# Kernel optimization log

Measured on AMD Instinct MI355X. Metric: run time of the kernel, lower is better.

The kernel has to match this reference:

```python
import jax, jax.numpy as jnp
import numpy as np

NUM_HEADS = 12
HEAD_DIM = 64
DIM = NUM_HEADS * HEAD_DIM  # 768
WIN = 14
REL = 2 * WIN - 1  # 27


def setup_inputs() -> dict:
    key = jax.random.key(0)
    ks = jax.random.split(key, 7)
    B, N = 256, WIN * WIN
    return {
        "x": jax.random.normal(ks[0], (B, N, DIM), dtype=jnp.float32),
        "qkv_w": jax.random.normal(ks[1], (3 * DIM, DIM), dtype=jnp.float32) * 0.02,
        "qkv_b": jnp.zeros((3 * DIM,), dtype=jnp.float32),
        "rel_pos_h": jax.random.normal(ks[2], (REL, HEAD_DIM), dtype=jnp.float32) * 0.02,
        "rel_pos_w": jax.random.normal(ks[3], (REL, HEAD_DIM), dtype=jnp.float32) * 0.02,
        "proj_w": jax.random.normal(ks[4], (DIM, DIM), dtype=jnp.float32) * 0.02,
        "proj_b": jnp.zeros((DIM,), dtype=jnp.float32),
        "H": WIN,
        "W": WIN,
    }


def _rel_pos_bias(q, rel_pos_h, rel_pos_w, H, W):
    # q: [B, heads, H*W, d] (already scaled). q_shape == k_shape == (H, W), ratios == 1.
    dist_h = jnp.arange(H)[:, None] - jnp.arange(H)[None, :] + (H - 1)  # [H, H]
    dist_w = jnp.arange(W)[:, None] - jnp.arange(W)[None, :] + (W - 1)  # [W, W]
    Rh = rel_pos_h[dist_h]  # [H, H, d]
    Rw = rel_pos_w[dist_w]  # [W, W, d]
    B, nh = q.shape[0], q.shape[1]
    r_q = q.reshape(B, nh, H, W, q.shape[-1])
    rel_h = jnp.einsum("bnhwd,hkd->bnhwk", r_q, Rh)  # [B, nh, H, W, Hk]
    rel_w = jnp.einsum("bnhwd,wkd->bnhwk", r_q, Rw)  # [B, nh, H, W, Wk]
    return rel_h[..., :, None] + rel_w[..., None, :]  # [B, nh, H, W, Hk, Wk]


def reference(x, qkv_w, qkv_b, rel_pos_h, rel_pos_w, proj_w, proj_b, H, W):
    B, N, C = x.shape
    d = C // NUM_HEADS
    scale = d ** -0.5
    qkv = x @ qkv_w.T + qkv_b  # [B, N, 3C]
    qkv = qkv.reshape(B, N, 3, NUM_HEADS, d).transpose(2, 0, 3, 1, 4)
    q, k, v = qkv[0], qkv[1], qkv[2]  # [B, nh, N, d]
    q = q * scale
    attn = jnp.einsum("bhqd,bhkd->bhqk", q, k)  # [B, nh, N, N]
    bias = _rel_pos_bias(q, rel_pos_h, rel_pos_w, H, W)
    attn = (attn.reshape(B, NUM_HEADS, H, W, H, W) + bias).reshape(B, NUM_HEADS, N, N)
    attn = jax.nn.softmax(attn, axis=-1)
    out = jnp.einsum("bhqk,bhkd->bhqd", attn, v)  # [B, nh, N, d]
    out = out.transpose(0, 2, 1, 3).reshape(B, N, C)
    return out @ proj_w.T + proj_b
```

## Files before the change

kernel.cpp:

```cpp
#include <hip/hip_runtime.h>
#include <stdint.h>


typedef __attribute__((ext_vector_type(8))) short bf16x8;
typedef __attribute__((ext_vector_type(4))) float f32x4;
typedef __attribute__((ext_vector_type(4))) unsigned int u32x4;
typedef unsigned short u16;
typedef unsigned int u32;

__device__ __forceinline__ u16 f2bf(float f) {
  u32 x = __float_as_uint(f);
  x += 0x7fffu + ((x >> 16) & 1u);
  return (u16)(x >> 16);
}

__device__ __forceinline__ u32 pack2bf(float a, float b) {
  return (u32)f2bf(a) | ((u32)f2bf(b) << 16);
}

__device__ __forceinline__ void gload_lds16(const void* g, void* l) {
  __builtin_amdgcn_global_load_lds(
      (__attribute__((address_space(1))) void*)g,
      (__attribute__((address_space(3))) void*)l, 16, 0, 0);
}

__global__ __launch_bounds__(256) void cvt_bf16(const float* __restrict__ src,
                                                u16* __restrict__ dst, int n4) {
  int i = blockIdx.x * 256 + threadIdx.x;
  if (i < n4) {
    float4 f = ((const float4*)src)[i];
    uint2 p;
    p.x = pack2bf(f.x, f.y);
    p.y = pack2bf(f.z, f.w);
    ((uint2*)dst)[i] = p;
  }
}

__device__ __forceinline__ void stage8(const u16* pA, const u16* pB,
                                       char* dstA, int k0) {
#pragma unroll
  for (int i = 0; i < 4; i++)
    gload_lds16(pA + (size_t)i * 49152 + k0, dstA + i * 8192);
#pragma unroll
  for (int i = 0; i < 4; i++)
    gload_lds16(pB + (size_t)i * 49152 + k0, dstA + 32768 + i * 8192);
}

template <int MODE, int NT>
__global__ __launch_bounds__(512, 2) void gemm256(
    const u16* __restrict__ A, const u16* __restrict__ W,
    const float* __restrict__ bias, u16* __restrict__ qb, u16* __restrict__ kb,
    u16* __restrict__ vb, float* __restrict__ outf) {
  __shared__ char lds[131072];

  const int t = threadIdx.x;
  const int lane = t & 63, wv = t >> 6;
  const int quad = lane >> 4, l15 = lane & 15;
  const int wm = wv >> 2, wn = wv & 3;

  const u32 nwg = gridDim.x;
  const u32 wg = blockIdx.x;
  const u32 qd = nwg >> 3, rm = nwg & 7;
  const u32 xcd = wg & 7, loc = wg >> 3;
  const u32 swz = (xcd < rm) ? (xcd * (qd + 1) + loc)
                             : (rm * (qd + 1) + (xcd - rm) * qd + loc);
  const int mtile = swz / NT;
  const int ntile = (int)swz - mtile * NT;
  const int m0 = mtile << 8, n0 = ntile << 8;

  const int srow = t >> 3;
  const int scol = ((t & 7) ^ (srow & 7)) << 3;
  const u16* pA = A + (size_t)(m0 + srow) * 768 + scol;
  const u16* pB = W + (size_t)(n0 + srow) * 768 + scol;
  char* sdst = lds + t * 16;

  const int swz0 = ((quad) ^ (l15 & 7)) << 4;
  const int swz1 = ((4 + quad) ^ (l15 & 7)) << 4;
  const int arow = (wm * 128 + l15) * 128;
  const int brow = 32768 + (wn * 64 + l15) * 128;

  f32x4 acc[8][4];
#pragma unroll
  for (int i = 0; i < 8; i++)
#pragma unroll
    for (int j = 0; j < 4; j++) acc[i][j] = (f32x4){0.f, 0.f, 0.f, 0.f};

  stage8(pA, pB, sdst, 0);
  asm volatile("s_waitcnt vmcnt(0)" ::: "memory");
  __builtin_amdgcn_s_barrier();

  bf16x8 af[4][2], bfr[4][2];
  for (int kt = 0; kt < 12; ++kt) {
    char* bufc = lds + ((kt & 1) << 16);
    char* nsdst = sdst + (((kt & 1) ^ 1) << 16);
    const int k0n = (kt + 1) << 6;

#pragma unroll
    for (int mf = 0; mf < 4; mf++) {
      af[mf][0] = *(const bf16x8*)(bufc + arow + mf * 2048 + swz0);
      af[mf][1] = *(const bf16x8*)(bufc + arow + mf * 2048 + swz1);
    }
#pragma unroll
    for (int nf = 0; nf < 2; nf++) {
      bfr[nf][0] = *(const bf16x8*)(bufc + brow + nf * 2048 + swz0);
      bfr[nf][1] = *(const bf16x8*)(bufc + brow + nf * 2048 + swz1);
    }
    if (kt < 11) stage8(pA, pB, nsdst, k0n);
    __builtin_amdgcn_s_barrier();
    asm volatile("s_waitcnt lgkmcnt(0)" ::: "memory");
    __builtin_amdgcn_s_setprio(1);
#pragma unroll
    for (int k = 0; k < 2; k++)
#pragma unroll
      for (int mf = 0; mf < 4; mf++)
#pragma unroll
        for (int nf = 0; nf < 2; nf++)
          acc[mf][nf] = __builtin_amdgcn_mfma_f32_16x16x32_bf16(
              af[mf][k], bfr[nf][k], acc[mf][nf], 0, 0, 0);
    __builtin_amdgcn_s_setprio(0);
    __builtin_amdgcn_s_barrier();

#pragma unroll
    for (int nf = 2; nf < 4; nf++) {
      bfr[nf][0] = *(const bf16x8*)(bufc + brow + nf * 2048 + swz0);
      bfr[nf][1] = *(const bf16x8*)(bufc + brow + nf * 2048 + swz1);
    }
    __builtin_amdgcn_s_barrier();
    asm volatile("s_waitcnt lgkmcnt(0)" ::: "memory");
    __builtin_amdgcn_s_setprio(1);
#pragma unroll
    for (int k = 0; k < 2; k++)
#pragma unroll
      for (int mf = 0; mf < 4; mf++)
#pragma unroll
        for (int nf = 2; nf < 4; nf++)
          acc[mf][nf] = __builtin_amdgcn_mfma_f32_16x16x32_bf16(
              af[mf][k], bfr[nf][k], acc[mf][nf], 0, 0, 0);
    __builtin_amdgcn_s_setprio(0);
    __builtin_amdgcn_s_barrier();

#pragma unroll
    for (int mf = 0; mf < 4; mf++) {
      af[mf][0] = *(const bf16x8*)(bufc + arow + (mf + 4) * 2048 + swz0);
      af[mf][1] = *(const bf16x8*)(bufc + arow + (mf + 4) * 2048 + swz1);
    }
    __builtin_amdgcn_s_barrier();
    asm volatile("s_waitcnt lgkmcnt(0)" ::: "memory");
    __builtin_amdgcn_s_setprio(1);
#pragma unroll
    for (int k = 0; k < 2; k++)
#pragma unroll
      for (int mf = 0; mf < 4; mf++)
#pragma unroll
        for (int nf = 0; nf < 2; nf++)
          acc[mf + 4][nf] = __builtin_amdgcn_mfma_f32_16x16x32_bf16(
              af[mf][k], bfr[nf][k], acc[mf + 4][nf], 0, 0, 0);
    __builtin_amdgcn_s_setprio(0);
    __builtin_amdgcn_s_barrier();

    __builtin_amdgcn_s_setprio(1);
#pragma unroll
    for (int k = 0; k < 2; k++)
#pragma unroll
      for (int mf = 0; mf < 4; mf++)
#pragma unroll
        for (int nf = 2; nf < 4; nf++)
          acc[mf + 4][nf] = __builtin_amdgcn_mfma_f32_16x16x32_bf16(
              af[mf][k], bfr[nf][k], acc[mf + 4][nf], 0, 0, 0);
    __builtin_amdgcn_s_setprio(0);
    asm volatile("s_waitcnt vmcnt(0)" ::: "memory");
    __builtin_amdgcn_s_barrier();
  }

  if (MODE == 0) {
    const int which = n0 / 768;
    u16* dst = (which == 0) ? qb : ((which == 1) ? kb : vb);
    const float sc = (which == 0) ? 0.125f : 1.0f;
    float bs[4];
    size_t hb[4];
#pragma unroll
    for (int nf = 0; nf < 4; nf++) {
      int n = n0 + wn * 64 + nf * 16 + l15;
      int cc = n - which * 768;
      bs[nf] = bias[n];
      hb[nf] = (size_t)(cc >> 6) * 12544 + (size_t)(cc & 63);
    }
#pragma unroll
    for (int mf = 0; mf < 8; mf++) {
#pragma unroll
      for (int r = 0; r < 4; r++) {
        int m = m0 + wm * 128 + mf * 16 + (quad << 2) + r;
        int bb = m / 196;
        int tok = m - bb * 196;
        size_t rb = (size_t)bb * 150528 + (size_t)tok * 64;
#pragma unroll
        for (int nf = 0; nf < 4; nf++)
          dst[rb + hb[nf]] = f2bf((acc[mf][nf][r] + bs[nf]) * sc);
      }
    }
  } else {
    float bs[4];
#pragma unroll
    for (int nf = 0; nf < 4; nf++)
      bs[nf] = bias[n0 + wn * 64 + nf * 16 + l15];
#pragma unroll
    for (int mf = 0; mf < 8; mf++) {
#pragma unroll
      for (int r = 0; r < 4; r++) {
        int m = m0 + wm * 128 + mf * 16 + (quad << 2) + r;
#pragma unroll
        for (int nf = 0; nf < 4; nf++)
          outf[(size_t)m * 768 + (n0 + wn * 64 + nf * 16 + l15)] =
              acc[mf][nf][r] + bs[nf];
      }
    }
  }
}

__global__ __launch_bounds__(256) void attn_fused(
    const u16* __restrict__ qbuf, const u16* __restrict__ kbuf,
    const u16* __restrict__ vbuf, const float* __restrict__ rel_h,
    const float* __restrict__ rel_w, u16* __restrict__ aout) {
  __shared__ u16 Vt[26 * 512];
  __shared__ float TL[4][2][28][16];

  const int t = threadIdx.x;
  const int bh = blockIdx.x;
  const int b = bh / 12, h = bh - b * 12;
  const int lane = t & 63, wv = t >> 6;
  const int quad = lane >> 4, l15 = lane & 15;
  const size_t base = (size_t)bh * (196 * 64);

  for (int c = t; c < 196 * 8; c += 256) {
    int row = c >> 3, seg = c & 7;
    uint4 vv = *(const uint4*)(vbuf + base + row * 64 + seg * 8);
    const u16* pv8 = (const u16*)&vv;
    u16* dst = Vt + (row >> 3) * 512 + (row & 7);
#pragma unroll
    for (int e = 0; e < 8; e++) dst[(seg * 8 + e) * 8] = pv8[e];
  }
  for (int i = t; i < 12 * 64; i += 256) {
    int k = 196 + (i >> 6), d = i & 63;
    Vt[(k >> 3) * 512 + d * 8 + (k & 7)] = 0;
  }

  bf16x8 brl[2][2][2];
#pragma unroll
  for (int half = 0; half < 2; half++) {
    const float* relp = half ? rel_w : rel_h;
#pragma unroll
    for (int nt = 0; nt < 2; nt++) {
      int ridx = nt * 16 + l15;
      if (ridx > 26) ridx = 26;
#pragma unroll
      for (int ks = 0; ks < 2; ks++) {
        const float* p = relp + ridx * 64 + ks * 32 + quad * 8;
        float4 f0 = *(const float4*)p;
        float4 f1 = *(const float4*)(p + 4);
        bf16x8 r;
        r[0] = (short)f2bf(f0.x); r[1] = (short)f2bf(f0.y);
        r[2] = (short)f2bf(f0.z); r[3] = (short)f2bf(f0.w);
        r[4] = (short)f2bf(f1.x); r[5] = (short)f2bf(f1.y);
        r[6] = (short)f2bf(f1.z); r[7] = (short)f2bf(f1.w);
        brl[half][nt][ks] = r;
      }
    }
  }
  __syncthreads();

  float (*TLh)[16] = TL[wv][0];
  float (*TLw)[16] = TL[wv][1];
  const u16* kB = kbuf + base;
  const u16* qB = qbuf + base;

  for (int qt = wv; qt < 13; qt += 4) {
    int qrl = qt * 16 + l15;
    if (qrl > 195) qrl = 195;
    bf16x8 aq0 = *(const bf16x8*)(qB + qrl * 64 + quad * 8);
    bf16x8 aq1 = *(const bf16x8*)(qB + qrl * 64 + 32 + quad * 8);
    const int hq = qrl / 14, wq = qrl - hq * 14;

#pragma unroll
    for (int half = 0; half < 2; half++) {
#pragma unroll
      for (int nt = 0; nt < 2; nt++) {
        f32x4 tc = (f32x4){0.f, 0.f, 0.f, 0.f};
        tc = __builtin_amdgcn_mfma_f32_16x16x32_bf16(brl[half][nt][0], aq0, tc, 0, 0, 0);
        tc = __builtin_amdgcn_mfma_f32_16x16x32_bf16(brl[half][nt][1], aq1, tc, 0, 0, 0);
#pragma unroll
        for (int r = 0; r < 4; r++) {
          int r27 = nt * 16 + quad * 4 + r;
          if (r27 < 27) TL[wv][half][r27][l15] = tc[r];
        }
      }
    }

    u32 pw2[13][2];
    float sm = 0.f;
#pragma unroll
    for (int kt = 0; kt < 13; kt++) {
      int keyl = kt * 16 + l15;
      int keyc = (keyl > 195) ? 195 : keyl;
      bf16x8 bk0 = *(const bf16x8*)(kB + keyc * 64 + quad * 8);
      bf16x8 bk1 = *(const bf16x8*)(kB + keyc * 64 + 32 + quad * 8);
      f32x4 s = (f32x4){0.f, 0.f, 0.f, 0.f};
      s = __builtin_amdgcn_mfma_f32_16x16x32_bf16(bk0, aq0, s, 0, 0, 0);
      s = __builtin_amdgcn_mfma_f32_16x16x32_bf16(bk1, aq1, s, 0, 0, 0);
      const int key0 = kt * 16 + quad * 4;
      const int hk0 = key0 / 14, wk0 = key0 - 14 * hk0;
      const bool valid = (kt < 12) || (quad == 0);
      float pr[4];
#pragma unroll
      for (int r = 0; r < 4; r++) {
        int cr = (wk0 + r >= 14) ? 1 : 0;
        int hk = hk0 + cr, wk = wk0 + r - 14 * cr;
        float v = s[r] + TLh[hq - hk + 13][l15] + TLw[wq - wk + 13][l15];
        float p = valid ? __expf(v) : 0.f;
        pr[r] = p;
        sm += p;
      }
      pw2[kt][0] = pack2bf(pr[0], pr[1]);
      pw2[kt][1] = pack2bf(pr[2], pr[3]);
    }
    sm += __shfl_xor(sm, 16, 64);
    sm += __shfl_xor(sm, 32, 64);
    const float inv = 1.0f / sm;

    f32x4 oacc[4];
#pragma unroll
    for (int dt = 0; dt < 4; dt++) oacc[dt] = (f32x4){0.f, 0.f, 0.f, 0.f};
    const int srcA = l15 + ((quad & 1) << 5);
    const bool hi = (quad >> 1) != 0;
#pragma unroll
    for (int st = 0; st < 7; st++) {
      u32 w0, w1, w2, w3;
      if (st < 6) {
        u32 a0 = __shfl(pw2[2 * st][0], srcA), b0 = __shfl(pw2[2 * st + 1][0], srcA);
        u32 a1 = __shfl(pw2[2 * st][1], srcA), b1 = __shfl(pw2[2 * st + 1][1], srcA);
        u32 a2 = __shfl(pw2[2 * st][0], srcA + 16), b2 = __shfl(pw2[2 * st + 1][0], srcA + 16);
        u32 a3 = __shfl(pw2[2 * st][1], srcA + 16), b3 = __shfl(pw2[2 * st + 1][1], srcA + 16);
        w0 = hi ? b0 : a0; w1 = hi ? b1 : a1;
        w2 = hi ? b2 : a2; w3 = hi ? b3 : a3;
      } else {
        u32 a0 = __shfl(pw2[12][0], srcA);
        u32 a1 = __shfl(pw2[12][1], srcA);
        u32 a2 = __shfl(pw2[12][0], srcA + 16);
        u32 a3 = __shfl(pw2[12][1], srcA + 16);
        w0 = hi ? 0u : a0; w1 = hi ? 0u : a1;
        w2 = hi ? 0u : a2; w3 = hi ? 0u : a3;
      }
      u32x4 pbw = (u32x4){w0, w1, w2, w3};
      bf16x8 pb = __builtin_bit_cast(bf16x8, pbw);
      const bool mvalid = (st < 6) || (quad < 2);
#pragma unroll
      for (int dt = 0; dt < 4; dt++) {
        bf16x8 av = (bf16x8){0, 0, 0, 0, 0, 0, 0, 0};
        if (mvalid)
          av = *(const bf16x8*)(Vt + (st * 4 + quad) * 512 + (dt * 16 + l15) * 8);
        oacc[dt] = __builtin_amdgcn_mfma_f32_16x16x32_bf16(av, pb, oacc[dt], 0, 0, 0);
      }
    }

    const int qrow = qt * 16 + l15;
    if (qrow < 196) {
      u16* op = aout + ((size_t)(b * 196 + qrow) * 12 + h) * 64;
#pragma unroll
      for (int dt = 0; dt < 4; dt++) {
        uint2 stv;
        stv.x = pack2bf(oacc[dt][0] * inv, oacc[dt][1] * inv);
        stv.y = pack2bf(oacc[dt][2] * inv, oacc[dt][3] * inv);
        *(uint2*)(op + dt * 16 + quad * 4) = stv;
      }
    }
  }
}

extern "C" void kernel_launch(void* const* d_in, const int* in_sizes, int n_in,
                              void* d_out, int out_size, void* d_ws, size_t ws_size,
                              hipStream_t stream) {
  (void)in_sizes; (void)n_in; (void)out_size; (void)ws_size;
  const float* x      = (const float*)d_in[0];
  const float* qkv_w  = (const float*)d_in[1];
  const float* qkv_b  = (const float*)d_in[2];
  const float* rel_h  = (const float*)d_in[3];
  const float* rel_w  = (const float*)d_in[4];
  const float* proj_w = (const float*)d_in[5];
  const float* proj_b = (const float*)d_in[6];
  float* out = (float*)d_out;

  char* ws = (char*)d_ws;
  u16* xbf  = (u16*)(ws);
  u16* qbuf = (u16*)(ws + 77070336);
  u16* kbuf = (u16*)(ws + 154140672);
  u16* vbuf = (u16*)(ws + 231211008);
  u16* wqb  = (u16*)(ws + 308281344);
  u16* wpb  = (u16*)(ws + 311820288);

  cvt_bf16<<<37632, 256, 0, stream>>>(x, xbf, 38535168 / 4);
  cvt_bf16<<<1728, 256, 0, stream>>>(qkv_w, wqb, 1769472 / 4);
  cvt_bf16<<<576, 256, 0, stream>>>(proj_w, wpb, 589824 / 4);

  gemm256<0, 9><<<1764, 512, 0, stream>>>(xbf, wqb, qkv_b, qbuf, kbuf, vbuf,
                                          nullptr);
  attn_fused<<<3072, 256, 0, stream>>>(qbuf, kbuf, vbuf, rel_h, rel_w, xbf);
  gemm256<1, 3><<<588, 512, 0, stream>>>(xbf, wpb, proj_b, nullptr, nullptr,
                                         nullptr, out);
}
```

Baseline: 991.3 us.

## Interleave score/exp with PV MFMA per key pair and rotate V transpose stores

Restructures the attention inner loop so each pair of 16-key tiles is scored, exponentiated, shuffled and immediately multiplied into the output accumulator. The old code first held all 13 tiles of packed probabilities in registers. This cuts the live register footprint (pw2[13][2]) and lets the score MFMAs overlap with the PV MFMAs. The last partial tile is peeled out with index clamping. Separately, the V transpose into LDS rotates the element order by segment, which is meant to reduce LDS bank conflicts on the scattered stores.

```diff
diff --git a/kernel.cpp b/kernel.cpp
--- a/kernel.cpp
+++ b/kernel.cpp
@@ -237,7 +237,10 @@
     const u16* pv8 = (const u16*)&vv;
     u16* dst = Vt + (row >> 3) * 512 + (row & 7);
 #pragma unroll
-    for (int e = 0; e < 8; e++) dst[(seg * 8 + e) * 8] = pv8[e];
+    for (int e = 0; e < 8; e++) {
+      int ee = (e + seg) & 7;
+      dst[(seg * 8 + ee) * 8] = pv8[ee];
+    }
   }
   for (int i = t; i < 12 * 64; i += 256) {
     int k = 196 + (i >> 6), d = i & 63;
@@ -295,71 +298,98 @@
       }
     }
 
-    u32 pw2[13][2];
+    f32x4 oacc[4];
+#pragma unroll
+    for (int dt = 0; dt < 4; dt++) oacc[dt] = (f32x4){0.f, 0.f, 0.f, 0.f};
     float sm = 0.f;
-#pragma unroll
-    for (int kt = 0; kt < 13; kt++) {
-      int keyl = kt * 16 + l15;
-      int keyc = (keyl > 195) ? 195 : keyl;
+    const int srcA = l15 + ((quad & 1) << 5);
+    const bool hi = (quad >> 1) != 0;
+
+#pragma unroll 2
+    for (int st = 0; st < 6; st++) {
+      u32 pw[2][2];
+#pragma unroll
+      for (int u = 0; u < 2; u++) {
+        const int kt = st * 2 + u;
+        const int keyl = kt * 16 + l15;
+        bf16x8 bk0 = *(const bf16x8*)(kB + keyl * 64 + quad * 8);
+        bf16x8 bk1 = *(const bf16x8*)(kB + keyl * 64 + 32 + quad * 8);
+        f32x4 s = (f32x4){0.f, 0.f, 0.f, 0.f};
+        s = __builtin_amdgcn_mfma_f32_16x16x32_bf16(bk0, aq0, s, 0, 0, 0);
+        s = __builtin_amdgcn_mfma_f32_16x16x32_bf16(bk1, aq1, s, 0, 0, 0);
+        const int key0 = kt * 16 + quad * 4;
+        const int hk0 = key0 / 14, wk0 = key0 - 14 * hk0;
+        float pr[4];
+#pragma unroll
+        for (int r = 0; r < 4; r++) {
+          int cr = (wk0 + r >= 14) ? 1 : 0;
+          int hk = hk0 + cr, wk = wk0 + r - 14 * cr;
+          float v = s[r] + TLh[hq - hk + 13][l15] + TLw[wq - wk + 13][l15];
+          float p = __expf(v);
+          pr[r] = p;
+          sm += p;
+        }
+        pw[u][0] = pack2bf(pr[0], pr[1]);
+        pw[u][1] = pack2bf(pr[2], pr[3]);
+      }
+      u32 a0 = __shfl(pw[0][0], srcA),      b0 = __shfl(pw[1][0], srcA);
+      u32 a1 = __shfl(pw[0][1], srcA),      b1 = __shfl(pw[1][1], srcA);
+      u32 a2 = __shfl(pw[0][0], srcA + 16), b2 = __shfl(pw[1][0], srcA + 16);
+      u32 a3 = __shfl(pw[0][1], srcA + 16), b3 = __shfl(pw[1][1], srcA + 16);
+      u32x4 pbw = (u32x4){hi ? b0 : a0, hi ? b1 : a1, hi ? b2 : a2, hi ? b3 : a3};
+      bf16x8 pb = __builtin_bit_cast(bf16x8, pbw);
+#pragma unroll
+      for (int dt = 0; dt < 4; dt++) {
+        bf16x8 av = *(const bf16x8*)(Vt + (st * 4 + quad) * 512 + (dt * 16 + l15) * 8);
+        oacc[dt] = __builtin_amdgcn_mfma_f32_16x16x32_bf16(av, pb, oacc[dt], 0, 0, 0);
+      }
+    }
+
+    {
+      const int keyl = 192 + l15;
+      const int keyc = (keyl > 195) ? 195 : keyl;
       bf16x8 bk0 = *(const bf16x8*)(kB + keyc * 64 + quad * 8);
       bf16x8 bk1 = *(const bf16x8*)(kB + keyc * 64 + 32 + quad * 8);
       f32x4 s = (f32x4){0.f, 0.f, 0.f, 0.f};
       s = __builtin_amdgcn_mfma_f32_16x16x32_bf16(bk0, aq0, s, 0, 0, 0);
       s = __builtin_amdgcn_mfma_f32_16x16x32_bf16(bk1, aq1, s, 0, 0, 0);
-      const int key0 = kt * 16 + quad * 4;
+      const int key0 = 192 + quad * 4;
       const int hk0 = key0 / 14, wk0 = key0 - 14 * hk0;
-      const bool valid = (kt < 12) || (quad == 0);
+      const bool valid = (quad == 0);
       float pr[4];
 #pragma unroll
       for (int r = 0; r < 4; r++) {
         int cr = (wk0 + r >= 14) ? 1 : 0;
         int hk = hk0 + cr, wk = wk0 + r - 14 * cr;
-        float v = s[r] + TLh[hq - hk + 13][l15] + TLw[wq - wk + 13][l15];
+        int ih = hq - hk + 13; ih = ih < 0 ? 0 : ih;
+        int iw = wq - wk + 13; iw = iw < 0 ? 0 : iw;
+        float v = s[r] + TLh[ih][l15] + TLw[iw][l15];
         float p = valid ? __expf(v) : 0.f;
         pr[r] = p;
         sm += p;
       }
-      pw2[kt][0] = pack2bf(pr[0], pr[1]);
-      pw2[kt][1] = pack2bf(pr[2], pr[3]);
-    }
+      u32 pw0 = pack2bf(pr[0], pr[1]);
+      u32 pw1 = pack2bf(pr[2], pr[3]);
+      const int srcA = l15 + ((quad & 1) << 5);
+      const bool hi = (quad >> 1) != 0;
+      u32 a0 = __shfl(pw0, srcA);
+      u32 a1 = __shfl(pw1, srcA);
+      u32 a2 = __shfl(pw0, srcA + 16);
+      u32 a3 = __shfl(pw1, srcA + 16);
+      u32x4 pbw = (u32x4){hi ? 0u : a0, hi ? 0u : a1, hi ? 0u : a2, hi ? 0u : a3};
+      bf16x8 pb = __builtin_bit_cast(bf16x8, pbw);
+#pragma unroll
+      for (int dt = 0; dt < 4; dt++) {
+        bf16x8 av = (bf16x8){0, 0, 0, 0, 0, 0, 0, 0};
+        if (quad < 2)
+          av = *(const bf16x8*)(Vt + (24 + quad) * 512 + (dt * 16 + l15) * 8);
+        oacc[dt] = __builtin_amdgcn_mfma_f32_16x16x32_bf16(av, pb, oacc[dt], 0, 0, 0);
+      }
+    }
+
     sm += __shfl_xor(sm, 16, 64);
     sm += __shfl_xor(sm, 32, 64);
     const float inv = 1.0f / sm;
-
-    f32x4 oacc[4];
-#pragma unroll
-    for (int dt = 0; dt < 4; dt++) oacc[dt] = (f32x4){0.f, 0.f, 0.f, 0.f};
-    const int srcA = l15 + ((quad & 1) << 5);
-    const bool hi = (quad >> 1) != 0;
-#pragma unroll
-    for (int st = 0; st < 7; st++) {
-      u32 w0, w1, w2, w3;
-      if (st < 6) {
-        u32 a0 = __shfl(pw2[2 * st][0], srcA), b0 = __shfl(pw2[2 * st + 1][0], srcA);
-        u32 a1 = __shfl(pw2[2 * st][1], srcA), b1 = __shfl(pw2[2 * st + 1][1], srcA);
-        u32 a2 = __shfl(pw2[2 * st][0], srcA + 16), b2 = __shfl(pw2[2 * st + 1][0], srcA + 16);
-        u32 a3 = __shfl(pw2[2 * st][1], srcA + 16), b3 = __shfl(pw2[2 * st + 1][1], srcA + 16);
-        w0 = hi ? b0 : a0; w1 = hi ? b1 : a1;
-        w2 = hi ? b2 : a2; w3 = hi ? b3 : a3;
-      } else {
-        u32 a0 = __shfl(pw2[12][0], srcA);
-        u32 a1 = __shfl(pw2[12][1], srcA);
-        u32 a2 = __shfl(pw2[12][0], srcA + 16);
-        u32 a3 = __shfl(pw2[12][1], srcA + 16);
-        w0 = hi ? 0u : a0; w1 = hi ? 0u : a1;
-        w2 = hi ? 0u : a2; w3 = hi ? 0u : a3;
-      }
-      u32x4 pbw = (u32x4){w0, w1, w2, w3};
-      bf16x8 pb = __builtin_bit_cast(bf16x8, pbw);
-      const bool mvalid = (st < 6) || (quad < 2);
-#pragma unroll
-      for (int dt = 0; dt < 4; dt++) {
-        bf16x8 av = (bf16x8){0, 0, 0, 0, 0, 0, 0, 0};
-        if (mvalid)
-          av = *(const bf16x8*)(Vt + (st * 4 + quad) * 512 + (dt * 16 + l15) * 8);
-        oacc[dt] = __builtin_amdgcn_mfma_f32_16x16x32_bf16(av, pb, oacc[dt], 0, 0, 0);
-      }
-    }
 
     const int qrow = qt * 16 + l15;
     if (qrow < 196) {
```

Result: faster. 846.3 us (-14.6%).
